# Kernel optimization log

Measured on AMD Instinct MI355X. Metric: run time of the kernel, lower is better.

The kernel has to match this reference:

```python
import jax, jax.numpy as jnp
import numpy as np

N = 100000
E = 1600000
C_IN = 32
HEADS = 4
C = 32          # per-head out channels
L = 3           # num layers = num_hidden_layers + 1
NEG_SLOPE = 0.2


def setup_inputs() -> dict:
    key = jax.random.key(0)
    ks = jax.random.split(key, 8)
    x = jax.random.normal(ks[0], (N, C_IN), dtype=jnp.float32)
    edge_index = jax.random.randint(ks[1], (2, E), 0, N, dtype=jnp.int64)
    edge_attr = jax.random.normal(ks[2], (E, 8), dtype=jnp.float32)  # unused by GATConv (edge_dim=None)
    scale = 1.0 / np.sqrt(C_IN)
    Ws = jax.random.normal(ks[3], (L, C_IN, HEADS * C), dtype=jnp.float32) * scale
    att_src = jax.random.normal(ks[4], (L, HEADS, C), dtype=jnp.float32) * scale
    att_dst = jax.random.normal(ks[5], (L, HEADS, C), dtype=jnp.float32) * scale
    bias = jnp.zeros((L, C), dtype=jnp.float32)
    return {"x": x, "edge_index": edge_index, "edge_attr": edge_attr,
            "Ws": Ws, "att_src": att_src, "att_dst": att_dst, "bias": bias}


def _gat_layer(x, src, dst, W, a_src, a_dst, b):
    # x: [N, C_in]; src/dst: [E'] (self-loops included); W: [C_in, H*C]
    h = (x @ W).reshape(N, HEADS, C)                      # [N, H, C]
    alpha_src = jnp.sum(h * a_src, axis=-1)               # [N, H]
    alpha_dst = jnp.sum(h * a_dst, axis=-1)               # [N, H]
    e = alpha_src[src] + alpha_dst[dst]                   # [E', H]
    e = jnp.where(e > 0, e, NEG_SLOPE * e)                # leaky_relu
    # segment softmax over incoming edges of each dst node
    m = jax.ops.segment_max(e, dst, num_segments=N)       # [N, H]
    ex = jnp.exp(e - m[dst])
    s = jax.ops.segment_sum(ex, dst, num_segments=N)      # [N, H]
    alpha = ex / (s[dst] + 1e-16)                         # [E', H]
    msg = h[src] * alpha[:, :, None]                      # [E', H, C]
    out = jax.ops.segment_sum(msg, dst, num_segments=N)   # [N, H, C]
    return out.mean(axis=1) + b                           # concat=False -> mean over heads, + bias


def reference(x, edge_index, edge_attr, Ws, att_src, att_dst, bias):
    # add self loops once (GATConv add_self_loops=True)
    loops = jnp.arange(N, dtype=edge_index.dtype)
    src = jnp.concatenate([edge_index[0], loops])
    dst = jnp.concatenate([edge_index[1], loops])
    # edge_attr unused: GATConv built without edge_dim.
    # Dropout layers are identity in eval mode.
    for l in range(L):
        x = _gat_layer(x, src, dst, Ws[l], att_src[l], att_dst[l], bias[l])
        x = jax.nn.elu(x)
    return x
```

## Files before the change

kernel.cpp:

```cpp
#include <hip/hip_runtime.h>
#include <hip/hip_bf16.h>
#include <hip/hip_fp16.h>
#include <cstdint>

#define NCHUNK 32
#define NRANGE 8
#define SCAT_PER 16


__global__ void __launch_bounds__(256)
k_hist_lds(const int* __restrict__ dstv, int E, int chunkSize, int n, int rangeSize,
           int* __restrict__ chist, int* __restrict__ rank) {
    __shared__ int lh[12800];
    int c = blockIdx.x & (NCHUNK - 1);
    int r = blockIdx.x / NCHUNK;
    int base = r * rangeSize;
    int rsz = min(rangeSize, n - base);
    if (rsz <= 0) return;
    int t = threadIdx.x;
    for (int i = t; i < rsz; i += 256) lh[i] = 0;
    __syncthreads();
    int e0 = c * chunkSize;
    int e1 = min(e0 + chunkSize, E);
    for (int i = e0 + t; i < e1; i += 256) {
        int d = dstv[i];
        unsigned rel = (unsigned)(d - base);
        if (rel < (unsigned)rsz) rank[i] = atomicAdd(&lh[rel], 1);
    }
    __syncthreads();
    int* out = chist + (size_t)c * n + base;
    for (int i = t; i < rsz; i += 256) out[i] = lh[i];
}

__global__ void k_chist_scan(int* __restrict__ chist, int n, int* __restrict__ deg) {
    int d = blockIdx.x * blockDim.x + threadIdx.x;
    if (d >= n) return;
    int sum = 0;
#pragma unroll
    for (int c = 0; c < NCHUNK; ++c) {
        int v = chist[(size_t)c * n + d];
        chist[(size_t)c * n + d] = sum;
        sum += v;
    }
    deg[d] = sum;
}

__global__ void k_scan1(const int* __restrict__ deg, int n, int* __restrict__ bsums) {
    __shared__ int s[256];
    int t = threadIdx.x;
    int i = blockIdx.x * 256 + t;
    int v = (i < n) ? deg[i] : 0;
    s[t] = v; __syncthreads();
    for (int off = 128; off > 0; off >>= 1) {
        if (t < off) s[t] += s[t + off];
        __syncthreads();
    }
    if (t == 0) bsums[blockIdx.x] = s[0];
}

__global__ void k_scan2(const int* __restrict__ bsums, int nb, int* __restrict__ boffs) {
    __shared__ int s[512];
    int t = threadIdx.x;
    int v = (t < nb) ? bsums[t] : 0;
    s[t] = v; __syncthreads();
    for (int off = 1; off < 512; off <<= 1) {
        int nv = (t >= off) ? s[t - off] : 0;
        __syncthreads();
        s[t] += nv;
        __syncthreads();
    }
    if (t < nb) boffs[t] = s[t] - v;
}

__global__ void k_scan3(const int* __restrict__ deg, int n, const int* __restrict__ boffs,
                        int* __restrict__ rowst) {
    __shared__ int s[256];
    int t = threadIdx.x;
    int i = blockIdx.x * 256 + t;
    int v = (i < n) ? deg[i] : 0;
    s[t] = v; __syncthreads();
    for (int off = 1; off < 256; off <<= 1) {
        int nv = (t >= off) ? s[t - off] : 0;
        __syncthreads();
        s[t] += nv;
        __syncthreads();
    }
    int incl = s[t] + boffs[blockIdx.x];
    if (i < n) {
        rowst[i] = incl - v;
        if (i == n - 1) rowst[n] = incl;
    }
}

__global__ void k_scatter(const int* __restrict__ src, const int* __restrict__ dst,
                          const int* __restrict__ rank, const int* __restrict__ rowst,
                          const int* __restrict__ chist, int n, int E, int chunkSize,
                          int blocksPerChunk, int* __restrict__ col) {
    int c = blockIdx.x / blocksPerChunk;
    int lb = blockIdx.x % blocksPerChunk;
    const int* cslice = chist + (size_t)c * n;
    int cbeg = c * chunkSize;
    int cend = min(cbeg + chunkSize, E);
    int base = cbeg + (lb * 256 + threadIdx.x) * SCAT_PER;
    if (base + SCAT_PER <= cend) {
        int4 d[4], s[4], r[4];
#pragma unroll
        for (int k = 0; k < 4; ++k) {
            d[k] = *reinterpret_cast<const int4*>(dst + base + k * 4);
            s[k] = *reinterpret_cast<const int4*>(src + base + k * 4);
            r[k] = *reinterpret_cast<const int4*>(rank + base + k * 4);
        }
        const int* dd = reinterpret_cast<const int*>(d);
        const int* ss = reinterpret_cast<const int*>(s);
        const int* rr = reinterpret_cast<const int*>(r);
        int p[16];
#pragma unroll
        for (int k = 0; k < 16; ++k) p[k] = rowst[dd[k]] + cslice[dd[k]] + rr[k];
#pragma unroll
        for (int k = 0; k < 16; ++k) col[p[k]] = ss[k];
    } else {
        for (int i = base; i < cend; ++i)
            col[rowst[dst[i]] + cslice[dst[i]] + rank[i]] = src[i];
    }
}


__device__ __forceinline__ float lane_bcast(float v, int k) {
    return __int_as_float(__builtin_amdgcn_readlane(__float_as_int(v), k));
}

__global__ void __launch_bounds__(256)
k_gemm_alpha(const float* __restrict__ x, const float* __restrict__ W,
             const float* __restrict__ a_src, const float* __restrict__ a_dst,
             __half* __restrict__ h16, float* __restrict__ alpha_src,
             float* __restrict__ alpha_dst, int n) {
    int lane = threadIdx.x & 63;
    int wave = threadIdx.x >> 6;
    int j2 = lane * 2;
    int nbase = blockIdx.x * 64 + wave * 16;

    float2 wr[32];
#pragma unroll
    for (int k = 0; k < 32; ++k)
        wr[k] = *reinterpret_cast<const float2*>(W + k * 128 + j2);
    float2 as2 = *reinterpret_cast<const float2*>(a_src + j2);
    float2 ad2 = *reinterpret_cast<const float2*>(a_dst + j2);

    float xr[16];
#pragma unroll
    for (int m = 0; m < 16; ++m) {
        int node = nbase + m;
        xr[m] = (node < n) ? x[(size_t)node * 32 + (lane & 31)] : 0.f;
    }

#pragma unroll
    for (int m = 0; m < 16; ++m) {
        int node = nbase + m;
        if (node >= n) continue;
        float acc0 = 0.f, acc1 = 0.f;
#pragma unroll
        for (int k = 0; k < 32; ++k) {
            float xv = lane_bcast(xr[m], k);
            acc0 += xv * wr[k].x;
            acc1 += xv * wr[k].y;
        }
        *reinterpret_cast<__half2*>(h16 + (size_t)node * 128 + j2) =
            __floats2half2_rn(acc0, acc1);
        float ps = acc0 * as2.x + acc1 * as2.y;
        float pd = acc0 * ad2.x + acc1 * ad2.y;
#pragma unroll
        for (int mm = 1; mm < 16; mm <<= 1) {
            ps += __shfl_xor(ps, mm, 64);
            pd += __shfl_xor(pd, mm, 64);
        }
        if ((lane & 15) == 0) {
            int head = lane >> 4;
            alpha_src[node * 4 + head] = ps;
            alpha_dst[node * 4 + head] = pd;
        }
    }
}

__device__ __forceinline__ float lrelu_exp(float e) {
    e = e > 0.f ? e : 0.2f * e;
    return __expf(e);
}

__global__ void k_agg(const __half* __restrict__ h16, const float* __restrict__ asrc,
                      const float* __restrict__ adst, const int* __restrict__ rowst,
                      const int* __restrict__ col, const float* __restrict__ bias,
                      float* __restrict__ out, int n) {
    int wid = (int)((blockIdx.x * (size_t)blockDim.x + threadIdx.x) >> 6);
    if (wid >= n) return;
    int lane = threadIdx.x & 63;
    int g = lane >> 4;
    int q = lane & 15;
    int head = q >> 2;
    float ad = adst[wid * 4 + head];

    float acc[8] = {0.f, 0.f, 0.f, 0.f, 0.f, 0.f, 0.f, 0.f};
    float s = 0.f;

    if (g == 0) {
        float w = lrelu_exp(asrc[wid * 4 + head] + ad);
        uint4 v = *reinterpret_cast<const uint4*>(h16 + (size_t)wid * 128 + q * 8);
        const __half2* hp = reinterpret_cast<const __half2*>(&v);
        s = w;
#pragma unroll
        for (int k = 0; k < 4; ++k) {
            float2 f = __half22float2(hp[k]);
            acc[2 * k]     += w * f.x;
            acc[2 * k + 1] += w * f.y;
        }
    }

    int beg = rowst[wid], end = rowst[wid + 1];
    int i = beg + g;
    for (; i + 4 < end; i += 8) {
        int s0 = col[i];
        int s1 = col[i + 4];
        float x0 = asrc[s0 * 4 + head];
        float x1 = asrc[s1 * 4 + head];
        uint4 v0 = *reinterpret_cast<const uint4*>(h16 + (size_t)s0 * 128 + q * 8);
        uint4 v1 = *reinterpret_cast<const uint4*>(h16 + (size_t)s1 * 128 + q * 8);
        float w0 = lrelu_exp(x0 + ad);
        float w1 = lrelu_exp(x1 + ad);
        s += w0 + w1;
        const __half2* h0 = reinterpret_cast<const __half2*>(&v0);
        const __half2* h1 = reinterpret_cast<const __half2*>(&v1);
#pragma unroll
        for (int k = 0; k < 4; ++k) {
            float2 f0 = __half22float2(h0[k]);
            float2 f1 = __half22float2(h1[k]);
            acc[2 * k]     += w0 * f0.x + w1 * f1.x;
            acc[2 * k + 1] += w0 * f0.y + w1 * f1.y;
        }
    }
    if (i < end) {
        int s0 = col[i];
        float w = lrelu_exp(asrc[s0 * 4 + head] + ad);
        uint4 v = *reinterpret_cast<const uint4*>(h16 + (size_t)s0 * 128 + q * 8);
        const __half2* hp = reinterpret_cast<const __half2*>(&v);
        s += w;
#pragma unroll
        for (int k = 0; k < 4; ++k) {
            float2 f = __half22float2(hp[k]);
            acc[2 * k]     += w * f.x;
            acc[2 * k + 1] += w * f.y;
        }
    }

    s += __shfl_xor(s, 16, 64);
    s += __shfl_xor(s, 32, 64);
#pragma unroll
    for (int k = 0; k < 8; ++k) {
        acc[k] += __shfl_xor(acc[k], 16, 64);
        acc[k] += __shfl_xor(acc[k], 32, 64);
    }
    float inv = 1.f / s;
#pragma unroll
    for (int k = 0; k < 8; ++k) acc[k] *= inv;
#pragma unroll
    for (int k = 0; k < 8; ++k) {
        acc[k] += __shfl_xor(acc[k], 4, 64);
        acc[k] += __shfl_xor(acc[k], 8, 64);
    }
    if (lane < 4) {
        float o[8];
#pragma unroll
        for (int k = 0; k < 8; ++k) {
            float v = acc[k] * 0.25f + bias[lane * 8 + k];
            o[k] = v > 0.f ? v : (__expf(v) - 1.f);
        }
        float4* op = reinterpret_cast<float4*>(&out[(size_t)wid * 32 + lane * 8]);
        op[0] = make_float4(o[0], o[1], o[2], o[3]);
        op[1] = make_float4(o[4], o[5], o[6], o[7]);
    }
}


extern "C" void kernel_launch(void* const* d_in, const int* in_sizes, int n_in,
                              void* d_out, int out_size, void* d_ws, size_t ws_size,
                              hipStream_t stream) {
    const float* x       = (const float*)d_in[0];
    const int*   ei      = (const int*)d_in[1];
    const float* Ws      = (const float*)d_in[3];
    const float* att_src = (const float*)d_in[4];
    const float* att_dst = (const float*)d_in[5];
    const float* bias    = (const float*)d_in[6];

    int N = in_sizes[0] / 32;
    int E = in_sizes[1] / 2;
    const int* srcv = ei;
    const int* dstv = ei + E;

    float* fws   = (float*)d_ws;
    __half* h16  = (__half*)fws;
    float* asrc  = (float*)(h16 + (size_t)N * 128);
    float* adst  = asrc + (size_t)N * 4;
    float* xbuf  = adst + (size_t)N * 4;
    int*   deg    = (int*)(xbuf + (size_t)N * 32);
    int*   rowst  = deg + N;
    int*   bsums  = rowst + N + 1;
    int*   boffs  = bsums + 512;
    int*   col    = boffs + 512;
    int*   rank   = col + E;
    int*   chist  = rank + E;

    int nb256 = (N + 255) / 256;
    int gemmBlocks = (N + 63) / 64;
    int rangeSize = (N + NRANGE - 1) / NRANGE;
    int chunkSize = (E + NCHUNK - 1) / NCHUNK;
    int blocksPerChunk = (chunkSize + 256 * SCAT_PER - 1) / (256 * SCAT_PER);

    k_hist_lds<<<NRANGE * NCHUNK, 256, 0, stream>>>(dstv, E, chunkSize, N, rangeSize,
                                                    chist, rank);
    k_chist_scan<<<nb256, 256, 0, stream>>>(chist, N, deg);
    k_scan1<<<nb256, 256, 0, stream>>>(deg, N, bsums);
    k_scan2<<<1, 512, 0, stream>>>(bsums, nb256, boffs);
    k_scan3<<<nb256, 256, 0, stream>>>(deg, N, boffs, rowst);
    k_scatter<<<NCHUNK * blocksPerChunk, 256, 0, stream>>>(
        srcv, dstv, rank, rowst, chist, N, E, chunkSize, blocksPerChunk, col);

    for (int l = 0; l < 3; ++l) {
        const float* xin = (l == 0) ? x : xbuf;
        float* xout = (l == 2) ? (float*)d_out : xbuf;
        k_gemm_alpha<<<gemmBlocks, 256, 0, stream>>>(
            xin, Ws + (size_t)l * 32 * 128, att_src + l * 128, att_dst + l * 128,
            h16, asrc, adst, N);
        k_agg<<<(N + 3) / 4, 256, 0, stream>>>(
            h16, asrc, adst, rowst, col, bias + l * 32, xout, N);
    }
}
```

Measured before the change: 452.6 us.

## Fuse layer-0 GEMM with destination histogram in one launch, widen histogram grid

The layer-0 feature GEMM/alpha kernel and the LDS destination histogram now run as separate block ranges of a single launch, so the independent GEMM work can overlap the histogram. The histogram grid changes to 16 ranges by 40 chunks with a smaller LDS array, and destination indices are read with vectorised int4 loads. The chunk size is rounded to a multiple of 8 to keep those loads aligned, and a single thread handles the tail. The risk is that the GEMM blocks' high register use and the histogram blocks' LDS compete for occupancy, and the larger grid re-reads the destination array more times.

After: 403.1 us. -11.0%, faster.

```diff
diff --git a/kernel.cpp b/kernel.cpp
--- a/kernel.cpp
+++ b/kernel.cpp
@@ -3,34 +3,11 @@
 #include <hip/hip_fp16.h>
 #include <cstdint>
 
-#define NCHUNK 32
-#define NRANGE 8
+#define NCHUNK 40
+#define NRANGE 16
+#define RSIZE_MAX 6400
 #define SCAT_PER 16
 
-
-__global__ void __launch_bounds__(256)
-k_hist_lds(const int* __restrict__ dstv, int E, int chunkSize, int n, int rangeSize,
-           int* __restrict__ chist, int* __restrict__ rank) {
-    __shared__ int lh[12800];
-    int c = blockIdx.x & (NCHUNK - 1);
-    int r = blockIdx.x / NCHUNK;
-    int base = r * rangeSize;
-    int rsz = min(rangeSize, n - base);
-    if (rsz <= 0) return;
-    int t = threadIdx.x;
-    for (int i = t; i < rsz; i += 256) lh[i] = 0;
-    __syncthreads();
-    int e0 = c * chunkSize;
-    int e1 = min(e0 + chunkSize, E);
-    for (int i = e0 + t; i < e1; i += 256) {
-        int d = dstv[i];
-        unsigned rel = (unsigned)(d - base);
-        if (rel < (unsigned)rsz) rank[i] = atomicAdd(&lh[rel], 1);
-    }
-    __syncthreads();
-    int* out = chist + (size_t)c * n + base;
-    for (int i = t; i < rsz; i += 256) out[i] = lh[i];
-}
 
 __global__ void k_chist_scan(int* __restrict__ chist, int n, int* __restrict__ deg) {
     int d = blockIdx.x * blockDim.x + threadIdx.x;
@@ -127,6 +104,94 @@
 
 __device__ __forceinline__ float lane_bcast(float v, int k) {
     return __int_as_float(__builtin_amdgcn_readlane(__float_as_int(v), k));
+}
+
+__global__ void __launch_bounds__(256)
+k_gemm_hist(const float* __restrict__ x, const float* __restrict__ W,
+            const float* __restrict__ a_src, const float* __restrict__ a_dst,
+            __half* __restrict__ h16, float* __restrict__ alpha_src,
+            float* __restrict__ alpha_dst, int n,
+            const int* __restrict__ dstv, int E, int chunkSize, int rangeSize,
+            int* __restrict__ chist, int* __restrict__ rank, int gemmBlocks) {
+    __shared__ int lh[RSIZE_MAX];
+    if ((int)blockIdx.x >= gemmBlocks) {
+        int b = blockIdx.x - gemmBlocks;
+        int c = b % NCHUNK;
+        int r = b / NCHUNK;
+        int base = r * rangeSize;
+        int rsz = min(rangeSize, n - base);
+        if (rsz <= 0) return;
+        int t = threadIdx.x;
+        for (int i = t; i < rsz; i += 256) lh[i] = 0;
+        __syncthreads();
+        int e0 = c * chunkSize;
+        int e1 = min(e0 + chunkSize, E);
+        for (int i = e0 + t * 8; i + 8 <= e1; i += 2048) {
+            int4 d0 = *reinterpret_cast<const int4*>(dstv + i);
+            int4 d1 = *reinterpret_cast<const int4*>(dstv + i + 4);
+            int dd[8] = {d0.x, d0.y, d0.z, d0.w, d1.x, d1.y, d1.z, d1.w};
+#pragma unroll
+            for (int k = 0; k < 8; ++k) {
+                unsigned rel = (unsigned)(dd[k] - base);
+                if (rel < (unsigned)rsz) rank[i + k] = atomicAdd(&lh[rel], 1);
+            }
+        }
+        if (t == 0) {
+            for (int i = e0 + ((e1 - e0) & ~7); i < e1; ++i) {
+                unsigned rel = (unsigned)(dstv[i] - base);
+                if (rel < (unsigned)rsz) rank[i] = atomicAdd(&lh[rel], 1);
+            }
+        }
+        __syncthreads();
+        int* outp = chist + (size_t)c * n + base;
+        for (int i = t; i < rsz; i += 256) outp[i] = lh[i];
+        return;
+    }
+    int lane = threadIdx.x & 63;
+    int wave = threadIdx.x >> 6;
+    int j2 = lane * 2;
+    int nbase = blockIdx.x * 64 + wave * 16;
+
+    float2 wr[32];
+#pragma unroll
+    for (int k = 0; k < 32; ++k)
+        wr[k] = *reinterpret_cast<const float2*>(W + k * 128 + j2);
+    float2 as2 = *reinterpret_cast<const float2*>(a_src + j2);
+    float2 ad2 = *reinterpret_cast<const float2*>(a_dst + j2);
+
+    float xr[16];
+#pragma unroll
+    for (int m = 0; m < 16; ++m) {
+        int node = nbase + m;
+        xr[m] = (node < n) ? x[(size_t)node * 32 + (lane & 31)] : 0.f;
+    }
+
+#pragma unroll
+    for (int m = 0; m < 16; ++m) {
+        int node = nbase + m;
+        if (node >= n) continue;
+        float acc0 = 0.f, acc1 = 0.f;
+#pragma unroll
+        for (int k = 0; k < 32; ++k) {
+            float xv = lane_bcast(xr[m], k);
+            acc0 += xv * wr[k].x;
+            acc1 += xv * wr[k].y;
+        }
+        *reinterpret_cast<__half2*>(h16 + (size_t)node * 128 + j2) =
+            __floats2half2_rn(acc0, acc1);
+        float ps = acc0 * as2.x + acc1 * as2.y;
+        float pd = acc0 * ad2.x + acc1 * ad2.y;
+#pragma unroll
+        for (int mm = 1; mm < 16; mm <<= 1) {
+            ps += __shfl_xor(ps, mm, 64);
+            pd += __shfl_xor(pd, mm, 64);
+        }
+        if ((lane & 15) == 0) {
+            int head = lane >> 4;
+            alpha_src[node * 4 + head] = ps;
+            alpha_dst[node * 4 + head] = pd;
+        }
+    }
 }
 
 __global__ void __launch_bounds__(256)
@@ -310,23 +375,25 @@
     int nb256 = (N + 255) / 256;
     int gemmBlocks = (N + 63) / 64;
     int rangeSize = (N + NRANGE - 1) / NRANGE;
-    int chunkSize = (E + NCHUNK - 1) / NCHUNK;
+    int chunkSize = (((E + NCHUNK - 1) / NCHUNK) + 7) & ~7;
     int blocksPerChunk = (chunkSize + 256 * SCAT_PER - 1) / (256 * SCAT_PER);
 
-    k_hist_lds<<<NRANGE * NCHUNK, 256, 0, stream>>>(dstv, E, chunkSize, N, rangeSize,
-                                                    chist, rank);
+    k_gemm_hist<<<gemmBlocks + NRANGE * NCHUNK, 256, 0, stream>>>(
+        x, Ws, att_src, att_dst, h16, asrc, adst, N,
+        dstv, E, chunkSize, rangeSize, chist, rank, gemmBlocks);
     k_chist_scan<<<nb256, 256, 0, stream>>>(chist, N, deg);
     k_scan1<<<nb256, 256, 0, stream>>>(deg, N, bsums);
     k_scan2<<<1, 512, 0, stream>>>(bsums, nb256, boffs);
     k_scan3<<<nb256, 256, 0, stream>>>(deg, N, boffs, rowst);
     k_scatter<<<NCHUNK * blocksPerChunk, 256, 0, stream>>>(
         srcv, dstv, rank, rowst, chist, N, E, chunkSize, blocksPerChunk, col);
-
-    for (int l = 0; l < 3; ++l) {
-        const float* xin = (l == 0) ? x : xbuf;
+    k_agg<<<(N + 3) / 4, 256, 0, stream>>>(
+        h16, asrc, adst, rowst, col, bias, (float*)xbuf, N);
+
+    for (int l = 1; l < 3; ++l) {
         float* xout = (l == 2) ? (float*)d_out : xbuf;
         k_gemm_alpha<<<gemmBlocks, 256, 0, stream>>>(
-            xin, Ws + (size_t)l * 32 * 128, att_src + l * 128, att_dst + l * 128,
+            xbuf, Ws + (size_t)l * 32 * 128, att_src + l * 128, att_dst + l * 128,
             h16, asrc, adst, N);
         k_agg<<<(N + 3) / 4, 256, 0, stream>>>(
             h16, asrc, adst, rowst, col, bias + l * 32, xout, N);
```
